# Performance work log

Measured on AMD Instinct MI355X. Metric: run time of the kernel, lower is better.

## Reference

```python
import jax, jax.numpy as jnp
import numpy as np

B, C, H, W = 8, 512, 64, 64
C8 = C // 8

def setup_inputs() -> dict:
    key = jax.random.key(0)
    ks = jax.random.split(key, 10)
    rn = lambda k, shape: jax.random.normal(k, shape, jnp.float32)
    return {
        "q": rn(ks[0], (B, C, H, W)),
        "k": rn(ks[1], (B, C, H, W)),
        "v": rn(ks[2], (B, C, H, W)),
        "Wq": rn(ks[3], (C8, C)) * 0.05,
        "bq": rn(ks[4], (C8,)) * 0.05,
        "Wk": rn(ks[5], (C8, C)) * 0.05,
        "bk": rn(ks[6], (C8,)) * 0.05,
        "Wv": rn(ks[7], (C, C)) * 0.05,
        "bv": rn(ks[8], (C,)) * 0.05,
        "gamma": rn(ks[9], ()) * 0.05,
    }

def reference(q, k, v, Wq, bq, Wk, bk, Wv, bv, gamma):
    _, _, Hh, Ww = q.shape
    # 1x1 convs == per-pixel channel matmuls
    pq = jnp.einsum('oc,bchw->bohw', Wq, q) + bq[None, :, None, None]
    pk = jnp.einsum('oc,bchw->bohw', Wk, k) + bk[None, :, None, None]
    pv = jnp.einsum('oc,bchw->bohw', Wv, v) + bv[None, :, None, None]
    # column (height-axis) attention energies, diagonal masked to -inf
    eH = jnp.einsum('bchw,bckw->bhwk', pq, pk)  # [B,H,W,H]
    diag_mask = jnp.where(jnp.eye(Hh, dtype=bool), -jnp.inf, 0.0)  # [H,H]
    eH = eH + diag_mask[None, :, None, :]
    # row (width-axis) attention energies
    eW = jnp.einsum('bchw,bchk->bhwk', pq, pk)  # [B,H,W,W]
    # joint softmax over concatenated H+W candidates
    att = jax.nn.softmax(jnp.concatenate([eH, eW], axis=3), axis=3)
    aH, aW = att[..., :Hh], att[..., Hh:]
    outH = jnp.einsum('bckw,bhwk->bchw', pv, aH)
    outW = jnp.einsum('bchk,bhwk->bchw', pv, aW)
    return gamma * (outH + outW) + v
```

## Files before the change

### kernel.cpp

```cpp
#include <hip/hip_runtime.h>
#include <math.h>

#define Bz 8
#define Cc 512
#define Hh 64
#define Ww 64
#define HW 4096
#define BK 64
#define AS (BK + 4)
#define TS 68

typedef __attribute__((ext_vector_type(8))) short short8;
typedef __attribute__((ext_vector_type(4))) short short4v;
typedef __attribute__((ext_vector_type(4))) float floatx4;

__device__ inline unsigned short f2bf(float x) {
    unsigned u = __float_as_uint(x);
    return (unsigned short)((u + 0x7FFFu + ((u >> 16) & 1u)) >> 16);
}
__device__ inline float b2f(unsigned short h) {
    return __uint_as_float(((unsigned)h) << 16);
}
__device__ inline short8 ld8(const unsigned short* p) {
    short4v a = *(const short4v*)p;
    short4v b = *(const short4v*)(p + 4);
    short8 r;
    r[0]=a[0]; r[1]=a[1]; r[2]=a[2]; r[3]=a[3];
    r[4]=b[0]; r[5]=b[1]; r[6]=b[2]; r[7]=b[3];
    return r;
}
__device__ inline short8 ld8s(const unsigned short* base, int row, int koct) {
    return ld8(base + row * TS + (((koct ^ (row & 7))) << 3));
}

__global__ __launch_bounds__(256) void wconv_kernel(
    const float* __restrict__ Wq, const float* __restrict__ Wk,
    const float* __restrict__ Wv, unsigned short* __restrict__ wsc)
{
    const int i = blockIdx.x * 256 + threadIdx.x;
    if (i < 32768) {
        float x = Wq[i];
        unsigned short h = f2bf(x);
        wsc[i] = h;
        wsc[32768 + i] = f2bf(x - b2f(h));
    } else if (i < 65536) {
        int j = i - 32768;
        float x = Wk[j];
        unsigned short h = f2bf(x);
        wsc[65536 + j] = h;
        wsc[98304 + j] = f2bf(x - b2f(h));
    } else {
        int j = i - 65536;
        wsc[131072 + j] = f2bf(Wv[j]);
    }
}

template<int BN, bool SPLIT, bool BF16OUT>
__global__ __launch_bounds__(256) void proj_mfma_kernel(
    const float* __restrict__ in0, const float* __restrict__ in1,
    const unsigned short* __restrict__ Wh0, const unsigned short* __restrict__ Wh1,
    const unsigned short* __restrict__ Wl0, const unsigned short* __restrict__ Wl1,
    const float* __restrict__ bias0, const float* __restrict__ bias1,
    int COUT, float* __restrict__ out0, float* __restrict__ out1,
    unsigned short* __restrict__ out16)
{
    constexpr int NS = SPLIT ? 2 : 1;
    constexpr int NT = BN / 32;
    __shared__ unsigned short Ah[NS][128][AS];
    __shared__ unsigned short Bh[NS][BN][AS];
    const int sel = blockIdx.z >> 3;
    const int b   = blockIdx.z & 7;
    const float* __restrict__ in = sel ? in1 : in0;
    const unsigned short* __restrict__ Wh = sel ? Wh1 : Wh0;
    const unsigned short* __restrict__ Wl = sel ? Wl1 : Wl0;
    const float* __restrict__ bias = sel ? bias1 : bias0;
    float* __restrict__ outT = sel ? out1 : out0;

    const int t = threadIdx.x, lane = t & 63, wv = t >> 6;
    const int p0 = blockIdx.x * 128, o0 = blockIdx.y * BN;
    const float* __restrict__ inb = in + (size_t)b * Cc * HW + p0;

    const int wm = (wv & 1) * 64;
    const int wn = (wv >> 1) * (BN / 2);

    floatx4 acc[4][NT];
#pragma unroll
    for (int i = 0; i < 4; ++i)
#pragma unroll
        for (int j = 0; j < NT; ++j) acc[i][j] = (floatx4)0.f;

    const int ap = t & 127;
    const int aoct0 = t >> 7;

    for (int kt = 0; kt < Cc / BK; ++kt) {
        const int c0 = kt * BK;
        __syncthreads();
#pragma unroll
        for (int r = 0; r < 4; ++r) {
            const int oct = aoct0 + r * 2;
            const float* src = inb + (size_t)(c0 + oct * 8) * HW + ap;
            float x[8];
#pragma unroll
            for (int j = 0; j < 8; ++j) x[j] = src[(size_t)j * HW];
            unsigned short h[8];
#pragma unroll
            for (int j = 0; j < 8; ++j) h[j] = f2bf(x[j]);
            *(ushort4*)&Ah[0][ap][oct * 8]     = make_ushort4(h[0], h[1], h[2], h[3]);
            *(ushort4*)&Ah[0][ap][oct * 8 + 4] = make_ushort4(h[4], h[5], h[6], h[7]);
            if constexpr (SPLIT) {
                unsigned short l[8];
#pragma unroll
                for (int j = 0; j < 8; ++j) l[j] = f2bf(x[j] - b2f(h[j]));
                *(ushort4*)&Ah[1][ap][oct * 8]     = make_ushort4(l[0], l[1], l[2], l[3]);
                *(ushort4*)&Ah[1][ap][oct * 8 + 4] = make_ushort4(l[4], l[5], l[6], l[7]);
            }
        }
#pragma unroll
        for (int r = 0; r < BN * 8 / 256; ++r) {
            const int task = t + 256 * r;
            const int o = task >> 3, oct = task & 7;
            const unsigned short* src = Wh + (size_t)(o0 + o) * Cc + c0 + oct * 8;
            ushort4 w0 = *(const ushort4*)src;
            ushort4 w1 = *(const ushort4*)(src + 4);
            *(ushort4*)&Bh[0][o][oct * 8]     = w0;
            *(ushort4*)&Bh[0][o][oct * 8 + 4] = w1;
            if constexpr (SPLIT) {
                const unsigned short* srcl = Wl + (size_t)(o0 + o) * Cc + c0 + oct * 8;
                ushort4 l0 = *(const ushort4*)srcl;
                ushort4 l1 = *(const ushort4*)(srcl + 4);
                *(ushort4*)&Bh[1][o][oct * 8]     = l0;
                *(ushort4*)&Bh[1][o][oct * 8 + 4] = l1;
            }
        }
        __syncthreads();
#pragma unroll
        for (int ks = 0; ks < 2; ++ks) {
            const int col = ks * 32 + (lane >> 4) * 8;
            short8 af[4], al[4];
#pragma unroll
            for (int mt = 0; mt < 4; ++mt) {
                const int row = wm + mt * 16 + (lane & 15);
                af[mt] = ld8(&Ah[0][row][col]);
                if constexpr (SPLIT) al[mt] = ld8(&Ah[1][row][col]);
            }
            short8 bfr[NT], blr[NT];
#pragma unroll
            for (int nt = 0; nt < NT; ++nt) {
                const int row = wn + nt * 16 + (lane & 15);
                bfr[nt] = ld8(&Bh[0][row][col]);
                if constexpr (SPLIT) blr[nt] = ld8(&Bh[1][row][col]);
            }
#pragma unroll
            for (int mt = 0; mt < 4; ++mt)
#pragma unroll
                for (int nt = 0; nt < NT; ++nt) {
                    acc[mt][nt] = __builtin_amdgcn_mfma_f32_16x16x32_bf16(
                        af[mt], bfr[nt], acc[mt][nt], 0, 0, 0);
                    if constexpr (SPLIT) {
                        acc[mt][nt] = __builtin_amdgcn_mfma_f32_16x16x32_bf16(
                            al[mt], bfr[nt], acc[mt][nt], 0, 0, 0);
                        acc[mt][nt] = __builtin_amdgcn_mfma_f32_16x16x32_bf16(
                            af[mt], blr[nt], acc[mt][nt], 0, 0, 0);
                    }
                }
        }
    }
    const int oc = lane & 15, quad = lane >> 4;
#pragma unroll
    for (int nt = 0; nt < NT; ++nt) {
        const int o = o0 + wn + nt * 16 + oc;
        const float bs = bias[o];
#pragma unroll
        for (int mt = 0; mt < 4; ++mt) {
#pragma unroll
            for (int r = 0; r < 4; ++r) {
                const int p = p0 + wm + mt * 16 + quad * 4 + r;
                if constexpr (BF16OUT) {
                    out16[((size_t)b * HW + p) * COUT + o] = f2bf(acc[mt][nt][r] + bs);
                } else {
                    outT[((size_t)b * HW + p) * COUT + o] = acc[mt][nt][r] + bs;
                }
            }
        }
    }
}

__global__ __launch_bounds__(256) void scores_kernel(
    const float* __restrict__ pqT, const float* __restrict__ pkT,
    float* __restrict__ S)
{
    const int x    = blockIdx.x;
    const int b    = blockIdx.y;
    const int mode = blockIdx.z;
    __shared__ float Q[64][65];
    __shared__ float K[64][65];
    for (int idx = threadIdx.x; idx < 4096; idx += 256) {
        int r = idx >> 6, c = idx & 63;
        int p = mode ? (x * Ww + r) : (r * Ww + x);
        size_t g = ((size_t)b * HW + p) * 64 + c;
        Q[r][c] = pqT[g];
        K[r][c] = pkT[g];
    }
    __syncthreads();
    const int qr = threadIdx.x >> 2;
    const int k0 = (threadIdx.x & 3) * 16;
    float acc[16];
#pragma unroll
    for (int j = 0; j < 16; ++j) acc[j] = 0.f;
#pragma unroll 4
    for (int c = 0; c < 64; ++c) {
        float qv = Q[qr][c];
#pragma unroll
        for (int j = 0; j < 16; ++j)
            acc[j] = fmaf(qv, K[k0 + j][c], acc[j]);
    }
    size_t o = mode ? (((size_t)(b * Hh + x) * Ww + qr) * 128 + 64 + k0)
                    : (((size_t)(b * Hh + qr) * Ww + x) * 128 + k0);
#pragma unroll
    for (int j = 0; j < 16; ++j) S[o + j] = acc[j];
}

__global__ __launch_bounds__(256) void softmax_kernel(
    const float* __restrict__ S, unsigned short* __restrict__ Abf)
{
    const int wave = threadIdx.x >> 6;
    const int lane = threadIdx.x & 63;
    const size_t row = (size_t)blockIdx.x * 4 + wave;
    const int h = (int)((row / Ww) % Hh);
    const float* p = S + row * 128;
    float s0 = p[lane], s1 = p[lane + 64];
    if (lane == h) s0 = -INFINITY;
    float m = fmaxf(s0, s1);
#pragma unroll
    for (int off = 32; off > 0; off >>= 1) m = fmaxf(m, __shfl_xor(m, off));
    float e0 = __expf(s0 - m), e1 = __expf(s1 - m);
    float s = e0 + e1;
#pragma unroll
    for (int off = 32; off > 0; off >>= 1) s += __shfl_xor(s, off);
    float inv = 1.0f / s;
    Abf[row * 128 + lane]      = f2bf(e0 * inv);
    Abf[row * 128 + 64 + lane] = f2bf(e1 * inv);
}

__global__ __launch_bounds__(256) void outH_mfma_kernel(
    const unsigned short* __restrict__ Abf, const unsigned short* __restrict__ pvT16,
    unsigned short* __restrict__ TH16)
{
    const int w = blockIdx.x;
    const int ctg = blockIdx.y;
    const int b = blockIdx.z;
    const int t = threadIdx.x, lane = t & 63, wv = t >> 6;
    const int l15 = lane & 15, h4 = lane >> 4;
    __shared__ unsigned short A[64 * TS];
    __shared__ unsigned short Pt[64 * TS];

    {
        const int rr = t >> 2, kq = t & 3;
        const unsigned short* src = Abf + ((((size_t)b * Hh + rr) * Ww + w) << 7) + kq * 16;
        ushort4 a0 = *(const ushort4*)(src);
        ushort4 a1 = *(const ushort4*)(src + 4);
        ushort4 a2 = *(const ushort4*)(src + 8);
        ushort4 a3 = *(const ushort4*)(src + 12);
        const int sw = (rr & 7) << 3;
        const int q0 = rr * TS + (((kq * 2) << 3) ^ sw);
        const int q1 = rr * TS + (((kq * 2 + 1) << 3) ^ sw);
        *(ushort4*)&A[q0] = a0; *(ushort4*)&A[q0 + 4] = a1;
        *(ushort4*)&A[q1] = a2; *(ushort4*)&A[q1 + 4] = a3;
    }
    __syncthreads();
    const int hm = (wv & 1) * 32, cn = (wv >> 1) * 32;
    short8 ah[2][2];
#pragma unroll
    for (int mt = 0; mt < 2; ++mt)
#pragma unroll
        for (int ks = 0; ks < 2; ++ks)
            ah[mt][ks] = ld8s(A, hm + mt * 16 + l15, ks * 4 + h4);

    for (int cc = 0; cc < 2; ++cc) {
        const int cbase = (ctg * 2 + cc) * 64;
        __syncthreads();
        {
            const int kp = t >> 3, co = t & 7, k0 = kp * 2;
            const unsigned short* s0 = pvT16 + (((size_t)b * HW + (size_t)k0 * Ww + w) << 9) + cbase + co * 8;
            const unsigned short* s1 = s0 + ((size_t)Ww << 9);
            short8 r0 = *(const short8*)s0;
            short8 r1 = *(const short8*)s1;
            const int oct = k0 >> 3, klo = k0 & 7;
#pragma unroll
            for (int j = 0; j < 8; ++j) {
                const int c = co * 8 + j;
                unsigned vv = (unsigned)(unsigned short)r0[j] | ((unsigned)(unsigned short)r1[j] << 16);
                *(unsigned*)&Pt[c * TS + (((oct ^ (c & 7)) << 3) + klo)] = vv;
            }
        }
        __syncthreads();
        floatx4 acc[2][2];
#pragma unroll
        for (int i = 0; i < 2; ++i)
#pragma unroll
            for (int j = 0; j < 2; ++j) acc[i][j] = (floatx4)0.f;
        short8 pf[2][2];
#pragma unroll
        for (int nt = 0; nt < 2; ++nt)
#pragma unroll
            for (int ks = 0; ks < 2; ++ks)
                pf[nt][ks] = ld8s(Pt, cn + nt * 16 + l15, ks * 4 + h4);
#pragma unroll
        for (int ks = 0; ks < 2; ++ks)
#pragma unroll
            for (int mt = 0; mt < 2; ++mt)
#pragma unroll
                for (int nt = 0; nt < 2; ++nt)
                    acc[mt][nt] = __builtin_amdgcn_mfma_f32_16x16x32_bf16(
                        ah[mt][ks], pf[nt][ks], acc[mt][nt], 0, 0, 0);
        const int quad = lane >> 4, oc = lane & 15;
#pragma unroll
        for (int mt = 0; mt < 2; ++mt)
#pragma unroll
            for (int nt = 0; nt < 2; ++nt) {
                const int c = cn + nt * 16 + oc;
                unsigned short* dst = TH16 + ((((size_t)b * Ww + w) * Hh) << 9) + cbase + c;
#pragma unroll
                for (int r = 0; r < 4; ++r) {
                    const int hh = hm + mt * 16 + quad * 4 + r;
                    dst[(size_t)hh << 9] = f2bf(acc[mt][nt][r]);
                }
            }
    }
}

__global__ __launch_bounds__(256) void outW_mfma_kernel(
    const unsigned short* __restrict__ Abf, const unsigned short* __restrict__ pvT16,
    const unsigned short* __restrict__ TH16, const float* __restrict__ vin,
    const float* __restrict__ gamma_p, float* __restrict__ out)
{
    const int h = blockIdx.x;
    const int ctg = blockIdx.y;
    const int b = blockIdx.z;
    const int t = threadIdx.x, lane = t & 63, wv = t >> 6;
    const int l15 = lane & 15, h4 = lane >> 4;
    const float gamma = gamma_p[0];
    __shared__ unsigned short A[64 * TS];
    __shared__ unsigned short Pt[64 * TS];
    __shared__ unsigned short T2[64 * TS];

    {
        const int rr = t >> 2, kq = t & 3;
        const unsigned short* src = Abf + ((((size_t)b * Hh + h) * Ww + rr) << 7) + 64 + kq * 16;
        ushort4 a0 = *(const ushort4*)(src);
        ushort4 a1 = *(const ushort4*)(src + 4);
        ushort4 a2 = *(const ushort4*)(src + 8);
        ushort4 a3 = *(const ushort4*)(src + 12);
        const int sw = (rr & 7) << 3;
        const int q0 = rr * TS + (((kq * 2) << 3) ^ sw);
        const int q1 = rr * TS + (((kq * 2 + 1) << 3) ^ sw);
        *(ushort4*)&A[q0] = a0; *(ushort4*)&A[q0 + 4] = a1;
        *(ushort4*)&A[q1] = a2; *(ushort4*)&A[q1 + 4] = a3;
    }
    __syncthreads();
    const int cm = (wv & 1) * 32, wn = (wv >> 1) * 32;
    short8 aw[2][2];
#pragma unroll
    for (int nt = 0; nt < 2; ++nt)
#pragma unroll
        for (int ks = 0; ks < 2; ++ks)
            aw[nt][ks] = ld8s(A, wn + nt * 16 + l15, ks * 4 + h4);

    for (int cc = 0; cc < 2; ++cc) {
        const int cbase = (ctg * 2 + cc) * 64;
        __syncthreads();
        {
            const int kp = t >> 3, co = t & 7, k0 = kp * 2;
            const unsigned short* s0 = pvT16 + (((size_t)b * HW + (size_t)h * Ww + k0) << 9) + cbase + co * 8;
            const unsigned short* s1 = s0 + 512;
            short8 r0 = *(const short8*)s0;
            short8 r1 = *(const short8*)s1;
            const int oct = k0 >> 3, klo = k0 & 7;
#pragma unroll
            for (int j = 0; j < 8; ++j) {
                const int c = co * 8 + j;
                unsigned vv = (unsigned)(unsigned short)r0[j] | ((unsigned)(unsigned short)r1[j] << 16);
                *(unsigned*)&Pt[c * TS + (((oct ^ (c & 7)) << 3) + klo)] = vv;
            }
        }
        {
            const int wr = t >> 2, cq = t & 3;
            const unsigned short* src = TH16 + ((((size_t)b * Ww + wr) * Hh + h) << 9) + cbase + cq * 16;
            short8 t0 = *(const short8*)src;
            short8 t1 = *(const short8*)(src + 8);
#pragma unroll
            for (int j = 0; j < 4; ++j) {
                unsigned va = (unsigned)(unsigned short)t0[2 * j] | ((unsigned)(unsigned short)t0[2 * j + 1] << 16);
                *(unsigned*)&T2[wr * TS + cq * 16 + 2 * j] = va;
                unsigned vb = (unsigned)(unsigned short)t1[2 * j] | ((unsigned)(unsigned short)t1[2 * j + 1] << 16);
                *(unsigned*)&T2[wr * TS + cq * 16 + 8 + 2 * j] = vb;
            }
        }
        __syncthreads();
        floatx4 acc[2][2];
#pragma unroll
        for (int i = 0; i < 2; ++i)
#pragma unroll
            for (int j = 0; j < 2; ++j) acc[i][j] = (floatx4)0.f;
        short8 pf[2][2];
#pragma unroll
        for (int mt = 0; mt < 2; ++mt)
#pragma unroll
            for (int ks = 0; ks < 2; ++ks)
                pf[mt][ks] = ld8s(Pt, cm + mt * 16 + l15, ks * 4 + h4);
#pragma unroll
        for (int ks = 0; ks < 2; ++ks)
#pragma unroll
            for (int mt = 0; mt < 2; ++mt)
#pragma unroll
                for (int nt = 0; nt < 2; ++nt)
                    acc[mt][nt] = __builtin_amdgcn_mfma_f32_16x16x32_bf16(
                        pf[mt][ks], aw[nt][ks], acc[mt][nt], 0, 0, 0);
        const int quad = lane >> 4, oc = lane & 15;
#pragma unroll
        for (int mt = 0; mt < 2; ++mt)
#pragma unroll
            for (int nt = 0; nt < 2; ++nt) {
                const int wcol = wn + nt * 16 + oc;
#pragma unroll
                for (int r = 0; r < 4; ++r) {
                    const int c = cm + mt * 16 + quad * 4 + r;
                    const float t2v = b2f(T2[wcol * TS + c]);
                    const size_t oa = ((size_t)(b * Cc + cbase + c) * HW) + (size_t)h * Ww + wcol;
                    out[oa] = gamma * (acc[mt][nt][r] + t2v) + vin[oa];
                }
            }
    }
}

extern "C" void kernel_launch(void* const* d_in, const int* in_sizes, int n_in,
                              void* d_out, int out_size, void* d_ws, size_t ws_size,
                              hipStream_t stream)
{
    const float* q   = (const float*)d_in[0];
    const float* k   = (const float*)d_in[1];
    const float* v   = (const float*)d_in[2];
    const float* Wq  = (const float*)d_in[3];
    const float* bq  = (const float*)d_in[4];
    const float* Wk  = (const float*)d_in[5];
    const float* bk  = (const float*)d_in[6];
    const float* Wv  = (const float*)d_in[7];
    const float* bv  = (const float*)d_in[8];
    const float* gam = (const float*)d_in[9];
    float* out = (float*)d_out;
    float* ws  = (float*)d_ws;

    float* pqT = ws;
    float* pkT = ws + 2097152;
    unsigned short* pvT16 = (unsigned short*)(ws + 4194304);
    float* S   = ws + 12582912;
    unsigned short* Abf  = (unsigned short*)(ws + 16777216);
    unsigned short* TH16 = (unsigned short*)(ws + 18874368);

    unsigned short* wsc = (unsigned short*)S;
    const unsigned short* Wqh = wsc;
    const unsigned short* Wql = wsc + 32768;
    const unsigned short* Wkh = wsc + 65536;
    const unsigned short* Wkl = wsc + 98304;
    const unsigned short* Wvh = wsc + 131072;

    wconv_kernel<<<1280, 256, 0, stream>>>(Wq, Wk, Wv, wsc);
    proj_mfma_kernel<64, true, false><<<dim3(32, 1, 16), 256, 0, stream>>>(
        q, k, Wqh, Wkh, Wql, Wkl, bq, bk, 64, pqT, pkT, nullptr);
    proj_mfma_kernel<128, false, true><<<dim3(32, 4, 8), 256, 0, stream>>>(
        v, v, Wvh, Wvh, Wvh, Wvh, bv, bv, 512, nullptr, nullptr, pvT16);
    scores_kernel<<<dim3(64, 8, 2), 256, 0, stream>>>(pqT, pkT, S);
    softmax_kernel<<<8192, 256, 0, stream>>>(S, Abf);
    outH_mfma_kernel<<<dim3(64, 4, 8), 256, 0, stream>>>(Abf, pvT16, TH16);
    outW_mfma_kernel<<<dim3(64, 4, 8), 256, 0, stream>>>(Abf, pvT16, TH16, v, gam, out);
}
```

Baseline: 341.0 us.

## Split projection kernel, vectorize input loads, and transpose K in scores

Replaces the templated projection kernel with two specialized kernels. The q/k projection now uses 64-pixel tiles, which doubles its grid, and both projections load input activations as float4 along the pixel axis instead of scalar strided loads. Occupancy hints are added through launch bounds. The scores kernel stores K transposed in shared memory so each thread reads float4 vectors instead of scalar strided values. The aim is to cut global load instruction count and LDS read cost, at the risk of bank conflicts from the new transposed shared-memory writes.

Measured after the change: 332.3 us. 2.6% less time.

```diff
diff --git a/kernel.cpp b/kernel.cpp
--- a/kernel.cpp
+++ b/kernel.cpp
@@ -55,19 +55,15 @@
     }
 }
 
-template<int BN, bool SPLIT, bool BF16OUT>
-__global__ __launch_bounds__(256) void proj_mfma_kernel(
+__global__ __launch_bounds__(256, 4) void qkproj_kernel(
     const float* __restrict__ in0, const float* __restrict__ in1,
     const unsigned short* __restrict__ Wh0, const unsigned short* __restrict__ Wh1,
     const unsigned short* __restrict__ Wl0, const unsigned short* __restrict__ Wl1,
     const float* __restrict__ bias0, const float* __restrict__ bias1,
-    int COUT, float* __restrict__ out0, float* __restrict__ out1,
-    unsigned short* __restrict__ out16)
-{
-    constexpr int NS = SPLIT ? 2 : 1;
-    constexpr int NT = BN / 32;
-    __shared__ unsigned short Ah[NS][128][AS];
-    __shared__ unsigned short Bh[NS][BN][AS];
+    float* __restrict__ out0, float* __restrict__ out1)
+{
+    __shared__ unsigned short Ah[2][64][AS];
+    __shared__ unsigned short Bh[2][64][AS];
     const int sel = blockIdx.z >> 3;
     const int b   = blockIdx.z & 7;
     const float* __restrict__ in = sel ? in1 : in0;
@@ -77,111 +73,174 @@
     float* __restrict__ outT = sel ? out1 : out0;
 
     const int t = threadIdx.x, lane = t & 63, wv = t >> 6;
-    const int p0 = blockIdx.x * 128, o0 = blockIdx.y * BN;
+    const int p0 = blockIdx.x * 64;
     const float* __restrict__ inb = in + (size_t)b * Cc * HW + p0;
 
-    const int wm = (wv & 1) * 64;
-    const int wn = (wv >> 1) * (BN / 2);
-
-    floatx4 acc[4][NT];
-#pragma unroll
-    for (int i = 0; i < 4; ++i)
-#pragma unroll
-        for (int j = 0; j < NT; ++j) acc[i][j] = (floatx4)0.f;
-
-    const int ap = t & 127;
-    const int aoct0 = t >> 7;
+    const int wm = (wv & 1) * 32;
+    const int wn = (wv >> 1) * 32;
+
+    floatx4 acc[2][2];
+#pragma unroll
+    for (int i = 0; i < 2; ++i)
+#pragma unroll
+        for (int j = 0; j < 2; ++j) acc[i][j] = (floatx4)0.f;
+
+    const int pq4 = t & 15;
+    const int cst = (t >> 4) * 4;
 
     for (int kt = 0; kt < Cc / BK; ++kt) {
         const int c0 = kt * BK;
         __syncthreads();
-#pragma unroll
-        for (int r = 0; r < 4; ++r) {
-            const int oct = aoct0 + r * 2;
-            const float* src = inb + (size_t)(c0 + oct * 8) * HW + ap;
-            float x[8];
-#pragma unroll
-            for (int j = 0; j < 8; ++j) x[j] = src[(size_t)j * HW];
-            unsigned short h[8];
-#pragma unroll
-            for (int j = 0; j < 8; ++j) h[j] = f2bf(x[j]);
-            *(ushort4*)&Ah[0][ap][oct * 8]     = make_ushort4(h[0], h[1], h[2], h[3]);
-            *(ushort4*)&Ah[0][ap][oct * 8 + 4] = make_ushort4(h[4], h[5], h[6], h[7]);
-            if constexpr (SPLIT) {
-                unsigned short l[8];
-#pragma unroll
-                for (int j = 0; j < 8; ++j) l[j] = f2bf(x[j] - b2f(h[j]));
-                *(ushort4*)&Ah[1][ap][oct * 8]     = make_ushort4(l[0], l[1], l[2], l[3]);
-                *(ushort4*)&Ah[1][ap][oct * 8 + 4] = make_ushort4(l[4], l[5], l[6], l[7]);
-            }
-        }
-#pragma unroll
-        for (int r = 0; r < BN * 8 / 256; ++r) {
+        float4 xq[4];
+#pragma unroll
+        for (int j = 0; j < 4; ++j)
+            xq[j] = *(const float4*)(inb + (size_t)(c0 + cst + j) * HW + (pq4 << 2));
+#pragma unroll
+        for (int jj = 0; jj < 4; ++jj) {
+            unsigned short h[4], l[4];
+#pragma unroll
+            for (int j = 0; j < 4; ++j) {
+                float xx = ((const float*)&xq[j])[jj];
+                h[j] = f2bf(xx);
+                l[j] = f2bf(xx - b2f(h[j]));
+            }
+            *(ushort4*)&Ah[0][(pq4 << 2) + jj][cst] = make_ushort4(h[0], h[1], h[2], h[3]);
+            *(ushort4*)&Ah[1][(pq4 << 2) + jj][cst] = make_ushort4(l[0], l[1], l[2], l[3]);
+        }
+#pragma unroll
+        for (int r = 0; r < 2; ++r) {
             const int task = t + 256 * r;
             const int o = task >> 3, oct = task & 7;
-            const unsigned short* src = Wh + (size_t)(o0 + o) * Cc + c0 + oct * 8;
-            ushort4 w0 = *(const ushort4*)src;
-            ushort4 w1 = *(const ushort4*)(src + 4);
-            *(ushort4*)&Bh[0][o][oct * 8]     = w0;
-            *(ushort4*)&Bh[0][o][oct * 8 + 4] = w1;
-            if constexpr (SPLIT) {
-                const unsigned short* srcl = Wl + (size_t)(o0 + o) * Cc + c0 + oct * 8;
-                ushort4 l0 = *(const ushort4*)srcl;
-                ushort4 l1 = *(const ushort4*)(srcl + 4);
-                *(ushort4*)&Bh[1][o][oct * 8]     = l0;
-                *(ushort4*)&Bh[1][o][oct * 8 + 4] = l1;
-            }
+            const unsigned short* srch = Wh + (size_t)o * Cc + c0 + oct * 8;
+            const unsigned short* srcl = Wl + (size_t)o * Cc + c0 + oct * 8;
+            *(ushort4*)&Bh[0][o][oct * 8]     = *(const ushort4*)srch;
+            *(ushort4*)&Bh[0][o][oct * 8 + 4] = *(const ushort4*)(srch + 4);
+            *(ushort4*)&Bh[1][o][oct * 8]     = *(const ushort4*)srcl;
+            *(ushort4*)&Bh[1][o][oct * 8 + 4] = *(const ushort4*)(srcl + 4);
         }
         __syncthreads();
 #pragma unroll
         for (int ks = 0; ks < 2; ++ks) {
             const int col = ks * 32 + (lane >> 4) * 8;
-            short8 af[4], al[4];
-#pragma unroll
-            for (int mt = 0; mt < 4; ++mt) {
+            short8 af[2], al[2], bfr[2], blr[2];
+#pragma unroll
+            for (int mt = 0; mt < 2; ++mt) {
                 const int row = wm + mt * 16 + (lane & 15);
                 af[mt] = ld8(&Ah[0][row][col]);
-                if constexpr (SPLIT) al[mt] = ld8(&Ah[1][row][col]);
-            }
-            short8 bfr[NT], blr[NT];
-#pragma unroll
-            for (int nt = 0; nt < NT; ++nt) {
+                al[mt] = ld8(&Ah[1][row][col]);
+            }
+#pragma unroll
+            for (int nt = 0; nt < 2; ++nt) {
                 const int row = wn + nt * 16 + (lane & 15);
                 bfr[nt] = ld8(&Bh[0][row][col]);
-                if constexpr (SPLIT) blr[nt] = ld8(&Bh[1][row][col]);
-            }
-#pragma unroll
-            for (int mt = 0; mt < 4; ++mt)
-#pragma unroll
-                for (int nt = 0; nt < NT; ++nt) {
+                blr[nt] = ld8(&Bh[1][row][col]);
+            }
+#pragma unroll
+            for (int mt = 0; mt < 2; ++mt)
+#pragma unroll
+                for (int nt = 0; nt < 2; ++nt) {
                     acc[mt][nt] = __builtin_amdgcn_mfma_f32_16x16x32_bf16(
                         af[mt], bfr[nt], acc[mt][nt], 0, 0, 0);
-                    if constexpr (SPLIT) {
-                        acc[mt][nt] = __builtin_amdgcn_mfma_f32_16x16x32_bf16(
-                            al[mt], bfr[nt], acc[mt][nt], 0, 0, 0);
-                        acc[mt][nt] = __builtin_amdgcn_mfma_f32_16x16x32_bf16(
-                            af[mt], blr[nt], acc[mt][nt], 0, 0, 0);
-                    }
+                    acc[mt][nt] = __builtin_amdgcn_mfma_f32_16x16x32_bf16(
+                        al[mt], bfr[nt], acc[mt][nt], 0, 0, 0);
+                    acc[mt][nt] = __builtin_amdgcn_mfma_f32_16x16x32_bf16(
+                        af[mt], blr[nt], acc[mt][nt], 0, 0, 0);
                 }
         }
     }
-    const int oc = lane & 15, quad = lane >> 4;
-#pragma unroll
-    for (int nt = 0; nt < NT; ++nt) {
+    const int oc = lane & 15, qd = lane >> 4;
+#pragma unroll
+    for (int nt = 0; nt < 2; ++nt) {
+        const int o = wn + nt * 16 + oc;
+        const float bs = bias[o];
+#pragma unroll
+        for (int mt = 0; mt < 2; ++mt)
+#pragma unroll
+            for (int r = 0; r < 4; ++r) {
+                const int p = p0 + wm + mt * 16 + qd * 4 + r;
+                outT[((size_t)b * HW + p) * 64 + o] = acc[mt][nt][r] + bs;
+            }
+    }
+}
+
+__global__ __launch_bounds__(256, 4) void vproj_kernel(
+    const float* __restrict__ in, const unsigned short* __restrict__ Wh,
+    const float* __restrict__ bias, unsigned short* __restrict__ out16)
+{
+    __shared__ unsigned short Ah[128][AS];
+    __shared__ unsigned short Bh[128][AS];
+    const int b = blockIdx.z;
+    const int t = threadIdx.x, lane = t & 63, wv = t >> 6;
+    const int p0 = blockIdx.x * 128, o0 = blockIdx.y * 128;
+    const float* __restrict__ inb = in + (size_t)b * Cc * HW + p0;
+    const int wm = (wv & 1) * 64, wn = (wv >> 1) * 64;
+
+    floatx4 acc[4][4];
+#pragma unroll
+    for (int i = 0; i < 4; ++i)
+#pragma unroll
+        for (int j = 0; j < 4; ++j) acc[i][j] = (floatx4)0.f;
+
+    const int pq4 = t & 31;
+    const int oct = t >> 5;
+
+    for (int kt = 0; kt < Cc / BK; ++kt) {
+        const int c0 = kt * BK;
+        __syncthreads();
+#pragma unroll
+        for (int half = 0; half < 2; ++half) {
+            float4 xq[4];
+#pragma unroll
+            for (int j = 0; j < 4; ++j)
+                xq[j] = *(const float4*)(inb + (size_t)(c0 + oct * 8 + half * 4 + j) * HW + (pq4 << 2));
+#pragma unroll
+            for (int jj = 0; jj < 4; ++jj) {
+                unsigned short h[4];
+#pragma unroll
+                for (int j = 0; j < 4; ++j) h[j] = f2bf(((const float*)&xq[j])[jj]);
+                *(ushort4*)&Ah[(pq4 << 2) + jj][oct * 8 + half * 4] =
+                    make_ushort4(h[0], h[1], h[2], h[3]);
+            }
+        }
+#pragma unroll
+        for (int r = 0; r < 4; ++r) {
+            const int task = t + 256 * r;
+            const int o = task >> 3, oc8 = task & 7;
+            const unsigned short* src = Wh + (size_t)(o0 + o) * Cc + c0 + oc8 * 8;
+            *(ushort4*)&Bh[o][oc8 * 8]     = *(const ushort4*)src;
+            *(ushort4*)&Bh[o][oc8 * 8 + 4] = *(const ushort4*)(src + 4);
+        }
+        __syncthreads();
+#pragma unroll
+        for (int ks = 0; ks < 2; ++ks) {
+            const int col = ks * 32 + (lane >> 4) * 8;
+            short8 af[4], bfr[4];
+#pragma unroll
+            for (int mt = 0; mt < 4; ++mt)
+                af[mt] = ld8(&Ah[wm + mt * 16 + (lane & 15)][col]);
+#pragma unroll
+            for (int nt = 0; nt < 4; ++nt)
+                bfr[nt] = ld8(&Bh[wn + nt * 16 + (lane & 15)][col]);
+#pragma unroll
+            for (int mt = 0; mt < 4; ++mt)
+#pragma unroll
+                for (int nt = 0; nt < 4; ++nt)
+                    acc[mt][nt] = __builtin_amdgcn_mfma_f32_16x16x32_bf16(
+                        af[mt], bfr[nt], acc[mt][nt], 0, 0, 0);
+        }
+    }
+    const int oc = lane & 15, qd = lane >> 4;
+#pragma unroll
+    for (int nt = 0; nt < 4; ++nt) {
         const int o = o0 + wn + nt * 16 + oc;
         const float bs = bias[o];
 #pragma unroll
-        for (int mt = 0; mt < 4; ++mt) {
+        for (int mt = 0; mt < 4; ++mt)
 #pragma unroll
             for (int r = 0; r < 4; ++r) {
-                const int p = p0 + wm + mt * 16 + quad * 4 + r;
-                if constexpr (BF16OUT) {
-                    out16[((size_t)b * HW + p) * COUT + o] = f2bf(acc[mt][nt][r] + bs);
-                } else {
-                    outT[((size_t)b * HW + p) * COUT + o] = acc[mt][nt][r] + bs;
-                }
-            }
-        }
+                const int p = p0 + wm + mt * 16 + qd * 4 + r;
+                out16[((size_t)b * HW + p) * 512 + o] = f2bf(acc[mt][nt][r] + bs);
+            }
     }
 }
 
@@ -193,13 +252,13 @@
     const int b    = blockIdx.y;
     const int mode = blockIdx.z;
     __shared__ float Q[64][65];
-    __shared__ float K[64][65];
+    __shared__ float Kt[64][68];
     for (int idx = threadIdx.x; idx < 4096; idx += 256) {
         int r = idx >> 6, c = idx & 63;
         int p = mode ? (x * Ww + r) : (r * Ww + x);
         size_t g = ((size_t)b * HW + p) * 64 + c;
         Q[r][c] = pqT[g];
-        K[r][c] = pkT[g];
+        Kt[c][r] = pkT[g];
     }
     __syncthreads();
     const int qr = threadIdx.x >> 2;
@@ -207,12 +266,29 @@
     float acc[16];
 #pragma unroll
     for (int j = 0; j < 16; ++j) acc[j] = 0.f;
-#pragma unroll 4
+#pragma unroll 2
     for (int c = 0; c < 64; ++c) {
-        float qv = Q[qr][c];
-#pragma unroll
-        for (int j = 0; j < 16; ++j)
-            acc[j] = fmaf(qv, K[k0 + j][c], acc[j]);
+        const float qv = Q[qr][c];
+        const float4 kv0 = *(const float4*)&Kt[c][k0];
+        const float4 kv1 = *(const float4*)&Kt[c][k0 + 4];
+        const float4 kv2 = *(const float4*)&Kt[c][k0 + 8];
+        const float4 kv3 = *(const float4*)&Kt[c][k0 + 12];
+        acc[0]  = fmaf(qv, kv0.x, acc[0]);
+        acc[1]  = fmaf(qv, kv0.y, acc[1]);
+        acc[2]  = fmaf(qv, kv0.z, acc[2]);
+        acc[3]  = fmaf(qv, kv0.w, acc[3]);
+        acc[4]  = fmaf(qv, kv1.x, acc[4]);
+        acc[5]  = fmaf(qv, kv1.y, acc[5]);
+        acc[6]  = fmaf(qv, kv1.z, acc[6]);
+        acc[7]  = fmaf(qv, kv1.w, acc[7]);
+        acc[8]  = fmaf(qv, kv2.x, acc[8]);
+        acc[9]  = fmaf(qv, kv2.y, acc[9]);
+        acc[10] = fmaf(qv, kv2.z, acc[10]);
+        acc[11] = fmaf(qv, kv2.w, acc[11]);
+        acc[12] = fmaf(qv, kv3.x, acc[12]);
+        acc[13] = fmaf(qv, kv3.y, acc[13]);
+        acc[14] = fmaf(qv, kv3.z, acc[14]);
+        acc[15] = fmaf(qv, kv3.w, acc[15]);
     }
     size_t o = mode ? (((size_t)(b * Hh + x) * Ww + qr) * 128 + 64 + k0)
                     : (((size_t)(b * Hh + qr) * Ww + x) * 128 + k0);
@@ -465,10 +541,9 @@
     const unsigned short* Wvh = wsc + 131072;
 
     wconv_kernel<<<1280, 256, 0, stream>>>(Wq, Wk, Wv, wsc);
-    proj_mfma_kernel<64, true, false><<<dim3(32, 1, 16), 256, 0, stream>>>(
-        q, k, Wqh, Wkh, Wql, Wkl, bq, bk, 64, pqT, pkT, nullptr);
-    proj_mfma_kernel<128, false, true><<<dim3(32, 4, 8), 256, 0, stream>>>(
-        v, v, Wvh, Wvh, Wvh, Wvh, bv, bv, 512, nullptr, nullptr, pvT16);
+    qkproj_kernel<<<dim3(64, 1, 16), 256, 0, stream>>>(
+        q, k, Wqh, Wkh, Wql, Wkl, bq, bk, pqT, pkT);
+    vproj_kernel<<<dim3(32, 4, 8), 256, 0, stream>>>(v, Wvh, bv, pvT16);
     scores_kernel<<<dim3(64, 8, 2), 256, 0, stream>>>(pqT, pkT, S);
     softmax_kernel<<<8192, 256, 0, stream>>>(S, Abf);
     outH_mfma_kernel<<<dim3(64, 4, 8), 256, 0, stream>>>(Abf, pvT16, TH16);
```
